# Kernel optimization log

Hardware: AMD Instinct MI355X
Metric: run time of the kernel (lower is better)

The kernel has to match this reference:

```python
import jax, jax.numpy as jnp
import numpy as np


def setup_inputs() -> dict:
    key = jax.random.key(0)
    k1, k2 = jax.random.split(key)
    # x stacks (real, imag) along dim 0: (2, B, C, G, H, W)
    x = jax.random.normal(k1, (2, 8, 512, 4, 32, 32), dtype=jnp.float32)
    # gamma is a learned scalar parameter (torch inits to 0; randomized here for a non-trivial path)
    gamma = jax.random.normal(k2, (1,), dtype=jnp.float32) * 0.1
    return {"x": x, "gamma": gamma}


def reference(x, gamma):
    xr, xi = x[0], x[1]                      # (B, C, G, H, W) real / imag parts
    B, C, G, H, W = xr.shape
    N = G * H * W
    qr = xr.reshape(B, C, N)                 # proj_query == proj_value (gp is None)
    qi = xi.reshape(B, C, N)

    # energy = q @ q^T (complex, no conjugation), shape (B, C, C)
    er = jnp.einsum('bcn,bdn->bcd', qr, qr) - jnp.einsum('bcn,bdn->bcd', qi, qi)
    ei = jnp.einsum('bcn,bdn->bcd', qr, qi) + jnp.einsum('bcn,bdn->bcd', qi, qr)

    # energy_new = complex(max(re), max(im)) - energy  (max over last dim, broadcast)
    er2 = jnp.max(er, axis=-1, keepdims=True) - er
    ei2 = jnp.max(ei, axis=-1, keepdims=True) - ei

    # SoftmaxCmplx: softmax over squared magnitude, output is real
    attention = jax.nn.softmax(er2 * er2 + ei2 * ei2, axis=-1)   # (B, C, C)

    # out = attention @ value (attention real, value complex)
    outr = jnp.einsum('bcd,bdn->bcn', attention, qr).reshape(B, C, G, H, W)
    outi = jnp.einsum('bcd,bdn->bcn', attention, qi).reshape(B, C, G, H, W)

    g = gamma[0]
    # cmplx(real, imag) -> stack along dim 0
    return jnp.stack([g * outr + xr, g * outi + xi], axis=0)
```

## Files before the change

### kernel.cpp

```cpp
#include <hip/hip_runtime.h>
#include <hip/hip_bf16.h>

#define B_ 8
#define C_ 512
#define N_ 4096
#define BK 32
#define NSPLIT 8
#define KCH (N_ / NSPLIT)
static const size_t PS = (size_t)B_ * C_ * C_;

typedef __bf16 bf16x8 __attribute__((ext_vector_type(8)));
typedef float f32x4 __attribute__((ext_vector_type(4)));

__device__ __constant__ unsigned char JCI[20] = {0,0,0,0,0,0,0,0, 1,1,1,1,1,1, 2,2,2,2, 3,3};
__device__ __constant__ unsigned char JDJ[20] = {0,1,2,3,4,5,6,7, 2,3,4,5,6,7, 4,5,6,7, 6,7};

__device__ __forceinline__ f32x4 mfma16(bf16x8 a, bf16x8 b, f32x4 c) {
    return __builtin_amdgcn_mfma_f32_16x16x32_bf16(a, b, c, 0, 0, 0);
}

__device__ __forceinline__ unsigned cvtpk_bf16(float lo, float hi) {
    unsigned r;
    asm("v_cvt_pk_bf16_f32 %0, %1, %2" : "=v"(r) : "v"(lo), "v"(hi));
    return r;
}

__device__ __forceinline__ void cvt_store4(const f32x4 v, __bf16* hp, __bf16* lp) {
    const unsigned u0 = __float_as_uint(v[0]), u1 = __float_as_uint(v[1]);
    const unsigned u2 = __float_as_uint(v[2]), u3 = __float_as_uint(v[3]);
    uint2 h, l;
    h.x = __builtin_amdgcn_perm(u1, u0, 0x07060302u);
    h.y = __builtin_amdgcn_perm(u3, u2, 0x07060302u);
    l.x = cvtpk_bf16(v[0] - __uint_as_float(u0 & 0xFFFF0000u),
                     v[1] - __uint_as_float(u1 & 0xFFFF0000u));
    l.y = cvtpk_bf16(v[2] - __uint_as_float(u2 & 0xFFFF0000u),
                     v[3] - __uint_as_float(u3 & 0xFFFF0000u));
    *(uint2*)hp = h;
    *(uint2*)lp = l;
}

__global__ __launch_bounds__(256, 2) void energy_kernel(const float* __restrict__ x,
                                                        float* __restrict__ pbuf) {
    __shared__ __align__(16) __bf16 Ah[128][40], Al[128][40], Chs[128][40], Cls[128][40];
    __shared__ __align__(16) __bf16 Bh[64][40], Bl[64][40], Dh[64][40], Dl[64][40];
    const int b = blockIdx.z, sp = blockIdx.y;
    const int cbase = JCI[blockIdx.x] * 128, dbase = JDJ[blockIdx.x] * 64;
    const int t = threadIdx.x, lane = t & 63, wave = t >> 6;
    const int m = lane & 15, quad = lane >> 4;
    const int wr = wave >> 1, wc = wave & 1;

    const float* qr = x + (size_t)b * C_ * N_;
    const float* qi = qr + (size_t)B_ * C_ * N_;
    const int kbase = sp * KCH;

    const int a_row = t >> 1, a_k = (t & 1) * 16;
    const int b_row = t >> 2, b_k = (t & 3) * 8;
    const float* agr = qr + (size_t)(cbase + a_row) * N_ + kbase + a_k;
    const float* agi = qi + (size_t)(cbase + a_row) * N_ + kbase + a_k;
    const float* bgr = qr + (size_t)(dbase + b_row) * N_ + kbase + b_k;
    const float* bgi = qi + (size_t)(dbase + b_row) * N_ + kbase + b_k;

    f32x4 accRR[4][2] = {}, accII[4][2] = {}, accEI[4][2] = {};
    f32x4 va[4], vc[4], vb[2], vd[2];

#define LOADK(kk)                                              \
    {                                                          \
        _Pragma("unroll") for (int u = 0; u < 4; ++u) {        \
            va[u] = *(const f32x4*)(agr + (kk) + u * 4);       \
            vc[u] = *(const f32x4*)(agi + (kk) + u * 4);       \
        }                                                      \
        _Pragma("unroll") for (int u = 0; u < 2; ++u) {        \
            vb[u] = *(const f32x4*)(bgr + (kk) + u * 4);       \
            vd[u] = *(const f32x4*)(bgi + (kk) + u * 4);       \
        }                                                      \
    }

    LOADK(0);
    for (int k0 = 0; k0 < KCH; k0 += BK) {
        __syncthreads();
#pragma unroll
        for (int u = 0; u < 4; ++u) {
            cvt_store4(va[u], &Ah[a_row][a_k + u * 4], &Al[a_row][a_k + u * 4]);
            cvt_store4(vc[u], &Chs[a_row][a_k + u * 4], &Cls[a_row][a_k + u * 4]);
        }
#pragma unroll
        for (int u = 0; u < 2; ++u) {
            cvt_store4(vb[u], &Bh[b_row][b_k + u * 4], &Bl[b_row][b_k + u * 4]);
            cvt_store4(vd[u], &Dh[b_row][b_k + u * 4], &Dl[b_row][b_k + u * 4]);
        }
        __syncthreads();

        const int kn = (k0 + BK < KCH) ? k0 + BK : 0;
        LOADK(kn);

        bf16x8 fBh[2], fBl[2], fDh[2], fDl[2];
#pragma unroll
        for (int j = 0; j < 2; ++j) {
            const int row = wc * 32 + j * 16 + m;
            fBh[j] = *(const bf16x8*)&Bh[row][quad * 8];
            fBl[j] = *(const bf16x8*)&Bl[row][quad * 8];
            fDh[j] = *(const bf16x8*)&Dh[row][quad * 8];
            fDl[j] = *(const bf16x8*)&Dl[row][quad * 8];
        }
#pragma unroll
        for (int i = 0; i < 4; ++i) {
            const int row = wr * 64 + i * 16 + m;
            const bf16x8 fAh = *(const bf16x8*)&Ah[row][quad * 8];
            const bf16x8 fAl = *(const bf16x8*)&Al[row][quad * 8];
            const bf16x8 fCh = *(const bf16x8*)&Chs[row][quad * 8];
            const bf16x8 fCl = *(const bf16x8*)&Cls[row][quad * 8];
#pragma unroll
            for (int j = 0; j < 2; ++j) {
                accRR[i][j] = mfma16(fAh, fBh[j], accRR[i][j]);
                accRR[i][j] = mfma16(fAh, fBl[j], accRR[i][j]);
                accRR[i][j] = mfma16(fAl, fBh[j], accRR[i][j]);
                accII[i][j] = mfma16(fCh, fDh[j], accII[i][j]);
                accII[i][j] = mfma16(fCh, fDl[j], accII[i][j]);
                accII[i][j] = mfma16(fCl, fDh[j], accII[i][j]);
                accEI[i][j] = mfma16(fAh, fDh[j], accEI[i][j]);
                accEI[i][j] = mfma16(fAh, fDl[j], accEI[i][j]);
                accEI[i][j] = mfma16(fAl, fDh[j], accEI[i][j]);
                accEI[i][j] = mfma16(fCh, fBh[j], accEI[i][j]);
                accEI[i][j] = mfma16(fCh, fBl[j], accEI[i][j]);
                accEI[i][j] = mfma16(fCl, fBh[j], accEI[i][j]);
            }
        }
    }
#undef LOADK

    float* per = pbuf + (size_t)(2 * sp) * PS + (size_t)b * C_ * C_;
    float* pei = per + PS;
#pragma unroll
    for (int i = 0; i < 4; ++i)
#pragma unroll
        for (int j = 0; j < 2; ++j) {
            const int c0 = cbase + wr * 64 + i * 16 + quad * 4;
            const int d = dbase + wc * 32 + j * 16 + m;
            const f32x4 e = accRR[i][j] - accII[i][j];
            const f32x4 f = accEI[i][j];
#pragma unroll
            for (int r = 0; r < 4; ++r) {
                __builtin_nontemporal_store(e[r], per + (size_t)(c0 + r) * C_ + d);
                __builtin_nontemporal_store(f[r], pei + (size_t)(c0 + r) * C_ + d);
            }
            __builtin_nontemporal_store(e, (f32x4*)(per + (size_t)d * C_ + c0));
            __builtin_nontemporal_store(f, (f32x4*)(pei + (size_t)d * C_ + c0));
        }
}

__device__ __forceinline__ float waveMax(float v) {
#pragma unroll
    for (int off = 32; off > 0; off >>= 1) v = fmaxf(v, __shfl_xor(v, off));
    return v;
}
__device__ __forceinline__ float waveSum(float v) {
#pragma unroll
    for (int off = 32; off > 0; off >>= 1) v += __shfl_xor(v, off);
    return v;
}

__global__ __launch_bounds__(256) void softmax_kernel(const float* __restrict__ pbuf,
                                                      __bf16* __restrict__ att) {
    __shared__ float buf[4];
    const int b = blockIdx.y, c = blockIdx.x, t = threadIdx.x;
    const int wave = t >> 6, lane = t & 63;
    const size_t rbase = ((size_t)(b * C_ + c)) * C_;

    float er0 = 0.f, er1 = 0.f, ei0 = 0.f, ei1 = 0.f;
#pragma unroll
    for (int s = 0; s < NSPLIT; ++s) {
        const float* per = pbuf + (size_t)(2 * s) * PS;
        const float* pei = per + PS;
        er0 += __builtin_nontemporal_load(per + rbase + t);
        er1 += __builtin_nontemporal_load(per + rbase + t + 256);
        ei0 += __builtin_nontemporal_load(pei + rbase + t);
        ei1 += __builtin_nontemporal_load(pei + rbase + t + 256);
    }

    float v = waveMax(fmaxf(er0, er1));
    if (lane == 0) buf[wave] = v;
    __syncthreads();
    const float mer = fmaxf(fmaxf(buf[0], buf[1]), fmaxf(buf[2], buf[3]));
    __syncthreads();

    v = waveMax(fmaxf(ei0, ei1));
    if (lane == 0) buf[wave] = v;
    __syncthreads();
    const float mei = fmaxf(fmaxf(buf[0], buf[1]), fmaxf(buf[2], buf[3]));
    __syncthreads();

    const float a0 = mer - er0, c0 = mei - ei0;
    const float a1 = mer - er1, c1 = mei - ei1;
    const float t0 = a0 * a0 + c0 * c0;
    const float t1 = a1 * a1 + c1 * c1;

    v = waveMax(fmaxf(t0, t1));
    if (lane == 0) buf[wave] = v;
    __syncthreads();
    const float mt = fmaxf(fmaxf(buf[0], buf[1]), fmaxf(buf[2], buf[3]));
    __syncthreads();

    const float e0 = expf(t0 - mt), e1 = expf(t1 - mt);
    v = waveSum(e0 + e1);
    if (lane == 0) buf[wave] = v;
    __syncthreads();
    const float s = buf[0] + buf[1] + buf[2] + buf[3];
    const float inv = 1.0f / s;

    att[rbase + t] = (__bf16)(e0 * inv);
    att[rbase + t + 256] = (__bf16)(e1 * inv);
}

__global__ __launch_bounds__(256, 2) void out_kernel(const float* __restrict__ x,
                                                     const __bf16* __restrict__ att,
                                                     const float* __restrict__ gamma,
                                                     float* __restrict__ out) {
    __shared__ __align__(16) unsigned Lr[64 * 20];
    __shared__ __align__(16) unsigned Li[64 * 20];
    const int b = blockIdx.z, ct = blockIdx.y, nt = blockIdx.x;
    const int t = threadIdx.x, lane = t & 63, wave = t >> 6;
    const int m = lane & 15, quad = lane >> 4;

    const float* qr = x + (size_t)b * C_ * N_;
    const float* qi = qr + (size_t)B_ * C_ * N_;
    const int cbase = ct * 256;
    const __bf16* arow = att + ((size_t)(b * C_ + cbase + wave * 16 + m)) * C_ + quad * 8;

    const int kp = t & 15;
    const int n4 = (t >> 4) * 4;
    const int n0 = nt * 64;

    f32x4 accr[4][4] = {}, acci[4][4] = {};
    f32x4 pr0, pr1, pi0, pi1;
    bf16x8 pa[4];

#define LOADO(kk)                                                                \
    {                                                                            \
        pr0 = *(const f32x4*)(qr + (size_t)((kk) + 2 * kp) * N_ + n0 + n4);      \
        pr1 = *(const f32x4*)(qr + (size_t)((kk) + 2 * kp + 1) * N_ + n0 + n4);  \
        pi0 = *(const f32x4*)(qi + (size_t)((kk) + 2 * kp) * N_ + n0 + n4);      \
        pi1 = *(const f32x4*)(qi + (size_t)((kk) + 2 * kp + 1) * N_ + n0 + n4);  \
        _Pragma("unroll") for (int h = 0; h < 4; ++h)                            \
            pa[h] = *(const bf16x8*)(arow + (size_t)(h * 64) * C_ + (kk));       \
    }

    LOADO(0);
    for (int kk = 0; kk < C_; kk += 32) {
        const f32x4 r0 = pr0, r1 = pr1, i0 = pi0, i1 = pi1;
        bf16x8 a[4];
#pragma unroll
        for (int h = 0; h < 4; ++h) a[h] = pa[h];
        __syncthreads();
#pragma unroll
        for (int u = 0; u < 4; ++u) {
            Lr[(n4 + u) * 20 + kp] = cvtpk_bf16(r0[u], r1[u]);
            Li[(n4 + u) * 20 + kp] = cvtpk_bf16(i0[u], i1[u]);
        }
        __syncthreads();

        const int kn = (kk + 32 < C_) ? kk + 32 : 0;
        LOADO(kn);
#pragma unroll
        for (int s = 0; s < 4; ++s) {
            const bf16x8 br = *(const bf16x8*)(&Lr[(s * 16 + m) * 20 + quad * 4]);
            const bf16x8 bi = *(const bf16x8*)(&Li[(s * 16 + m) * 20 + quad * 4]);
#pragma unroll
            for (int h = 0; h < 4; ++h) {
                accr[h][s] = mfma16(a[h], br, accr[h][s]);
                acci[h][s] = mfma16(a[h], bi, acci[h][s]);
            }
        }
    }
#undef LOADO

    const float g = gamma[0];
    float* outr = out + (size_t)b * C_ * N_;
    float* outi = outr + (size_t)B_ * C_ * N_;
#pragma unroll
    for (int h = 0; h < 4; ++h)
#pragma unroll
        for (int s = 0; s < 4; ++s)
#pragma unroll
            for (int r = 0; r < 4; ++r) {
                const int cc = cbase + h * 64 + wave * 16 + quad * 4 + r;
                const int nn = n0 + s * 16 + m;
                const size_t ix = (size_t)cc * N_ + nn;
                outr[ix] = g * accr[h][s][r] + qr[ix];
                outi[ix] = g * acci[h][s][r] + qi[ix];
            }
}

extern "C" void kernel_launch(void* const* d_in, const int* in_sizes, int n_in,
                              void* d_out, int out_size, void* d_ws, size_t ws_size,
                              hipStream_t stream) {
    const float* x = (const float*)d_in[0];
    const float* gamma = (const float*)d_in[1];
    float* out = (float*)d_out;

    float* pbuf = out;
    __bf16* att = (__bf16*)d_ws;

    energy_kernel<<<dim3(20, NSPLIT, B_), 256, 0, stream>>>(x, pbuf);
    softmax_kernel<<<dim3(C_, B_), 256, 0, stream>>>(pbuf, att);
    out_kernel<<<dim3(64, 2, 8), 256, 0, stream>>>(x, att, gamma, out);
}
```

Baseline: 471.6 us.

## Use 64x64 upper-triangular energy tiles with higher occupancy and plain memory ops

The energy kernel moves from 128x64 tiles (20 per batch and split) to 64x64 tiles covering the upper triangle (36 per batch and split). This cuts redundant work on diagonal tiles, adds more blocks, and raises the launch-bounds occupancy target from 2 to 3. The register-level prefetch of the next K slice is dropped, so loads now sit at the top of each iteration and must be hidden by occupancy instead. Nontemporal stores and loads on the partial-energy buffer become ordinary accesses, which may change cache behaviour for the softmax reads.

```diff
diff --git a/kernel.cpp b/kernel.cpp
--- a/kernel.cpp
+++ b/kernel.cpp
@@ -12,8 +12,10 @@
 typedef __bf16 bf16x8 __attribute__((ext_vector_type(8)));
 typedef float f32x4 __attribute__((ext_vector_type(4)));
 
-__device__ __constant__ unsigned char JCI[20] = {0,0,0,0,0,0,0,0, 1,1,1,1,1,1, 2,2,2,2, 3,3};
-__device__ __constant__ unsigned char JDJ[20] = {0,1,2,3,4,5,6,7, 2,3,4,5,6,7, 4,5,6,7, 6,7};
+__device__ __constant__ unsigned char JCI[36] = {
+    0,0,0,0,0,0,0,0, 1,1,1,1,1,1,1, 2,2,2,2,2,2, 3,3,3,3,3, 4,4,4,4, 5,5,5, 6,6, 7};
+__device__ __constant__ unsigned char JDJ[36] = {
+    0,1,2,3,4,5,6,7, 1,2,3,4,5,6,7, 2,3,4,5,6,7, 3,4,5,6,7, 4,5,6,7, 5,6,7, 6,7, 7};
 
 __device__ __forceinline__ f32x4 mfma16(bf16x8 a, bf16x8 b, f32x4 c) {
     return __builtin_amdgcn_mfma_f32_16x16x32_bf16(a, b, c, 0, 0, 0);
@@ -39,12 +41,12 @@
     *(uint2*)lp = l;
 }
 
-__global__ __launch_bounds__(256, 2) void energy_kernel(const float* __restrict__ x,
+__global__ __launch_bounds__(256, 3) void energy_kernel(const float* __restrict__ x,
                                                         float* __restrict__ pbuf) {
-    __shared__ __align__(16) __bf16 Ah[128][40], Al[128][40], Chs[128][40], Cls[128][40];
+    __shared__ __align__(16) __bf16 Ah[64][40], Al[64][40], Chs[64][40], Cls[64][40];
     __shared__ __align__(16) __bf16 Bh[64][40], Bl[64][40], Dh[64][40], Dl[64][40];
     const int b = blockIdx.z, sp = blockIdx.y;
-    const int cbase = JCI[blockIdx.x] * 128, dbase = JDJ[blockIdx.x] * 64;
+    const int cbase = JCI[blockIdx.x] * 64, dbase = JDJ[blockIdx.x] * 64;
     const int t = threadIdx.x, lane = t & 63, wave = t >> 6;
     const int m = lane & 15, quad = lane >> 4;
     const int wr = wave >> 1, wc = wave & 1;
@@ -53,45 +55,32 @@
     const float* qi = qr + (size_t)B_ * C_ * N_;
     const int kbase = sp * KCH;
 
-    const int a_row = t >> 1, a_k = (t & 1) * 16;
-    const int b_row = t >> 2, b_k = (t & 3) * 8;
-    const float* agr = qr + (size_t)(cbase + a_row) * N_ + kbase + a_k;
-    const float* agi = qi + (size_t)(cbase + a_row) * N_ + kbase + a_k;
-    const float* bgr = qr + (size_t)(dbase + b_row) * N_ + kbase + b_k;
-    const float* bgi = qi + (size_t)(dbase + b_row) * N_ + kbase + b_k;
-
-    f32x4 accRR[4][2] = {}, accII[4][2] = {}, accEI[4][2] = {};
-    f32x4 va[4], vc[4], vb[2], vd[2];
-
-#define LOADK(kk)                                              \
-    {                                                          \
-        _Pragma("unroll") for (int u = 0; u < 4; ++u) {        \
-            va[u] = *(const f32x4*)(agr + (kk) + u * 4);       \
-            vc[u] = *(const f32x4*)(agi + (kk) + u * 4);       \
-        }                                                      \
-        _Pragma("unroll") for (int u = 0; u < 2; ++u) {        \
-            vb[u] = *(const f32x4*)(bgr + (kk) + u * 4);       \
-            vd[u] = *(const f32x4*)(bgi + (kk) + u * 4);       \
-        }                                                      \
-    }
-
-    LOADK(0);
+    const int s_row = t >> 2, s_k = (t & 3) * 8;
+    const float* agr = qr + (size_t)(cbase + s_row) * N_ + kbase + s_k;
+    const float* agi = qi + (size_t)(cbase + s_row) * N_ + kbase + s_k;
+    const float* bgr = qr + (size_t)(dbase + s_row) * N_ + kbase + s_k;
+    const float* bgi = qi + (size_t)(dbase + s_row) * N_ + kbase + s_k;
+
+    f32x4 accRR[2][2] = {}, accII[2][2] = {}, accEI[2][2] = {};
+
     for (int k0 = 0; k0 < KCH; k0 += BK) {
-        __syncthreads();
-#pragma unroll
-        for (int u = 0; u < 4; ++u) {
-            cvt_store4(va[u], &Ah[a_row][a_k + u * 4], &Al[a_row][a_k + u * 4]);
-            cvt_store4(vc[u], &Chs[a_row][a_k + u * 4], &Cls[a_row][a_k + u * 4]);
-        }
+        f32x4 va[2], vc[2], vb[2], vd[2];
 #pragma unroll
         for (int u = 0; u < 2; ++u) {
-            cvt_store4(vb[u], &Bh[b_row][b_k + u * 4], &Bl[b_row][b_k + u * 4]);
-            cvt_store4(vd[u], &Dh[b_row][b_k + u * 4], &Dl[b_row][b_k + u * 4]);
-        }
-        __syncthreads();
-
-        const int kn = (k0 + BK < KCH) ? k0 + BK : 0;
-        LOADK(kn);
+            va[u] = *(const f32x4*)(agr + k0 + u * 4);
+            vc[u] = *(const f32x4*)(agi + k0 + u * 4);
+            vb[u] = *(const f32x4*)(bgr + k0 + u * 4);
+            vd[u] = *(const f32x4*)(bgi + k0 + u * 4);
+        }
+        __syncthreads();
+#pragma unroll
+        for (int u = 0; u < 2; ++u) {
+            cvt_store4(va[u], &Ah[s_row][s_k + u * 4], &Al[s_row][s_k + u * 4]);
+            cvt_store4(vc[u], &Chs[s_row][s_k + u * 4], &Cls[s_row][s_k + u * 4]);
+            cvt_store4(vb[u], &Bh[s_row][s_k + u * 4], &Bl[s_row][s_k + u * 4]);
+            cvt_store4(vd[u], &Dh[s_row][s_k + u * 4], &Dl[s_row][s_k + u * 4]);
+        }
+        __syncthreads();
 
         bf16x8 fBh[2], fBl[2], fDh[2], fDl[2];
 #pragma unroll
@@ -103,8 +92,8 @@
             fDl[j] = *(const bf16x8*)&Dl[row][quad * 8];
         }
 #pragma unroll
-        for (int i = 0; i < 4; ++i) {
-            const int row = wr * 64 + i * 16 + m;
+        for (int i = 0; i < 2; ++i) {
+            const int row = wr * 32 + i * 16 + m;
             const bf16x8 fAh = *(const bf16x8*)&Ah[row][quad * 8];
             const bf16x8 fAl = *(const bf16x8*)&Al[row][quad * 8];
             const bf16x8 fCh = *(const bf16x8*)&Chs[row][quad * 8];
@@ -126,25 +115,24 @@
             }
         }
     }
-#undef LOADK
 
     float* per = pbuf + (size_t)(2 * sp) * PS + (size_t)b * C_ * C_;
     float* pei = per + PS;
 #pragma unroll
-    for (int i = 0; i < 4; ++i)
+    for (int i = 0; i < 2; ++i)
 #pragma unroll
         for (int j = 0; j < 2; ++j) {
-            const int c0 = cbase + wr * 64 + i * 16 + quad * 4;
+            const int c0 = cbase + wr * 32 + i * 16 + quad * 4;
             const int d = dbase + wc * 32 + j * 16 + m;
             const f32x4 e = accRR[i][j] - accII[i][j];
             const f32x4 f = accEI[i][j];
 #pragma unroll
             for (int r = 0; r < 4; ++r) {
-                __builtin_nontemporal_store(e[r], per + (size_t)(c0 + r) * C_ + d);
-                __builtin_nontemporal_store(f[r], pei + (size_t)(c0 + r) * C_ + d);
-            }
-            __builtin_nontemporal_store(e, (f32x4*)(per + (size_t)d * C_ + c0));
-            __builtin_nontemporal_store(f, (f32x4*)(pei + (size_t)d * C_ + c0));
+                per[(size_t)(c0 + r) * C_ + d] = e[r];
+                pei[(size_t)(c0 + r) * C_ + d] = f[r];
+            }
+            *(f32x4*)(per + (size_t)d * C_ + c0) = e;
+            *(f32x4*)(pei + (size_t)d * C_ + c0) = f;
         }
 }
 
@@ -171,10 +159,10 @@
     for (int s = 0; s < NSPLIT; ++s) {
         const float* per = pbuf + (size_t)(2 * s) * PS;
         const float* pei = per + PS;
-        er0 += __builtin_nontemporal_load(per + rbase + t);
-        er1 += __builtin_nontemporal_load(per + rbase + t + 256);
-        ei0 += __builtin_nontemporal_load(pei + rbase + t);
-        ei1 += __builtin_nontemporal_load(pei + rbase + t + 256);
+        er0 += per[rbase + t];
+        er1 += per[rbase + t + 256];
+        ei0 += pei[rbase + t];
+        ei1 += pei[rbase + t + 256];
     }
 
     float v = waveMax(fmaxf(er0, er1));
@@ -300,7 +288,7 @@
     float* pbuf = out;
     __bf16* att = (__bf16*)d_ws;
 
-    energy_kernel<<<dim3(20, NSPLIT, B_), 256, 0, stream>>>(x, pbuf);
+    energy_kernel<<<dim3(36, NSPLIT, B_), 256, 0, stream>>>(x, pbuf);
     softmax_kernel<<<dim3(C_, B_), 256, 0, stream>>>(pbuf, att);
     out_kernel<<<dim3(64, 2, 8), 256, 0, stream>>>(x, att, gamma, out);
 }
```

After: 443.1 us. -6.0%, faster.
